# Performance work log

Hardware: AMD Instinct MI355X
Metric: run time of the kernel (lower is better)

Reference implementation:

```python
import jax, jax.numpy as jnp
import numpy as np

R_CUT = 2.5
N_BASIS = 8
BOX_SIZE = 10.0


def radial_encode(r, n, r_cut):
    """Gaussian radial basis on squared distance r: (...,) -> (..., n).
    Centers spread over [0, r_cut], width r_cut/n. (Helper source not given;
    this is the standard RBF encode used in such MD graph nets.)"""
    mu = jnp.linspace(0.0, r_cut, n, dtype=r.dtype)        # (n,)
    sigma = r_cut / n
    d = r[..., None] - mu                                   # (..., n)
    return jnp.exp(-0.5 * (d / sigma) ** 2)


def setup_inputs() -> dict:
    key = jax.random.key(0)
    k1, k2 = jax.random.split(key)
    batch, nodes, deg = 8, 20000, 32
    pos = jax.random.uniform(k1, (batch, nodes, 3), dtype=jnp.float32) * BOX_SIZE
    box = jnp.full((3,), BOX_SIZE, dtype=jnp.float32)
    nbr_idx = jax.random.randint(k2, (nodes, deg), 0, nodes, dtype=jnp.int64)
    return {"pos": pos, "box": box, "nbr_idx": nbr_idx}


def reference(pos, box, nbr_idx):
    # pos: (B, N, 3); box: (3,); nbr_idx: (N, deg)
    ang_box = box / (2.0 * jnp.pi)                          # (3,)
    # edges_read: gather neighbor positions -> (B, N, deg, 3)
    nbr_pos = pos[:, nbr_idx]                               # (B, N, deg, 3)
    edges = nbr_pos - pos[:, :, None]                       # relative displacement
    # periodic-box sin wrap
    edges = ang_box * jnp.sin(edges / ang_box)
    r = jnp.sum(edges ** 2, axis=-1)                        # (B, N, deg) squared dist
    x = radial_encode(r, N_BASIS, R_CUT)                    # (B, N, deg, 8)
    xv = x[..., None] * edges[..., None, :]                 # (B, N, deg, 8, 3) outer product
    # edges_reduce: sum over neighbor axis
    y = jnp.sum(x, axis=2)                                  # (B, N, 8)
    yv = jnp.sum(xv, axis=2)                                # (B, N, 8, 3)
    return (y, yv)
```

## Files before the change

### kernel.cpp

```cpp
#include <hip/hip_runtime.h>

static constexpr int BATCH = 8;
static constexpr int NODES = 20000;
static constexpr int DEG   = 32;
static constexpr int NB    = 8;

#if defined(__has_builtin) && __has_builtin(__builtin_amdgcn_exp2f)
#define EXP2F(x) __builtin_amdgcn_exp2f(x)
#else
#define EXP2F(x) exp2f(x)
#endif

static constexpr float C1 = -7.3865986f;
static constexpr float C2 = 5.2761417f;

__global__ __launch_bounds__(256)
void transpose_pos_kernel(const float* __restrict__ pos, float4* __restrict__ pos_t) {
    const int t = blockIdx.x * blockDim.x + threadIdx.x;
    if (t >= BATCH * NODES) return;
    const int b = t / NODES;
    const int i = t - b * NODES;
    pos_t[(size_t)i * BATCH + b] =
        make_float4(pos[3 * t + 0], pos[3 * t + 1], pos[3 * t + 2], 0.0f);
}

__global__ __launch_bounds__(256)
void graph_embed_kernel(const float4* __restrict__ pos_t,
                        const float* __restrict__ box,
                        const int*   __restrict__ nbr,
                        float* __restrict__ out)
{
    const int t = blockIdx.x * blockDim.x + threadIdx.x;
    if (t >= BATCH * NODES) return;
    const int i = t >> 3;
    const int b = t & 7;

    const float inv2pi = 0.15915494309189535f;
    const float ab0 = box[0] * inv2pi;
    const float ab1 = box[1] * inv2pi;
    const float ab2 = box[2] * inv2pi;
    const float ia0 = 1.0f / ab0;
    const float ia1 = 1.0f / ab1;
    const float ia2 = 1.0f / ab2;

    float h[NB - 1];
#pragma unroll
    for (int k = 0; k < NB - 1; ++k)
        h[k] = __expf(-0.6530612245f * (float)(2 * k + 1));

    const float4 p = pos_t[(size_t)i * BATCH + b];

    float y0[NB], v0[NB], v1[NB], v2[NB];
#pragma unroll
    for (int k = 0; k < NB; ++k) { y0[k] = 0.f; v0[k] = 0.f; v1[k] = 0.f; v2[k] = 0.f; }

    const int4* __restrict__ row = (const int4*)(nbr + (size_t)i * DEG);

    int4 idx = row[0];
    float4 q0 = pos_t[(size_t)idx.x * BATCH + b];
    float4 q1 = pos_t[(size_t)idx.y * BATCH + b];
    float4 q2 = pos_t[(size_t)idx.z * BATCH + b];
    float4 q3 = pos_t[(size_t)idx.w * BATCH + b];

#pragma unroll
    for (int grp = 0; grp < DEG / 4; ++grp) {
        float4 n0, n1, n2, n3;
        if (grp + 1 < DEG / 4) {
            const int4 nidx = row[grp + 1];
            n0 = pos_t[(size_t)nidx.x * BATCH + b];
            n1 = pos_t[(size_t)nidx.y * BATCH + b];
            n2 = pos_t[(size_t)nidx.z * BATCH + b];
            n3 = pos_t[(size_t)nidx.w * BATCH + b];
        }
        const float4 qs[4] = { q0, q1, q2, q3 };
#pragma unroll
        for (int jj = 0; jj < 4; ++jj) {
            const float4 q = qs[jj];
            const float e0 = ab0 * __sinf((q.x - p.x) * ia0);
            const float e1 = ab1 * __sinf((q.y - p.y) * ia1);
            const float e2 = ab2 * __sinf((q.z - p.z) * ia2);
            const float r  = fmaf(e0, e0, fmaf(e1, e1, e2 * e2));

            const float g = EXP2F(r * C2);
            float x = EXP2F(r * r * C1);
#pragma unroll
            for (int k = 0; k < NB; ++k) {
                y0[k] += x;
                v0[k] = fmaf(x, e0, v0[k]);
                v1[k] = fmaf(x, e1, v1[k]);
                v2[k] = fmaf(x, e2, v2[k]);
                if (k < NB - 1) x = x * g * h[k];
            }
        }
        q0 = n0; q1 = n1; q2 = n2; q3 = n3;
    }

    const size_t ot = (size_t)b * NODES + i;
    float* __restrict__ yptr = out + ot * NB;
    *(float4*)(yptr + 0) = make_float4(y0[0], y0[1], y0[2], y0[3]);
    *(float4*)(yptr + 4) = make_float4(y0[4], y0[5], y0[6], y0[7]);

    float* __restrict__ vptr = out + (size_t)BATCH * NODES * NB + ot * (NB * 3);
    *(float4*)(vptr +  0) = make_float4(v0[0], v1[0], v2[0], v0[1]);
    *(float4*)(vptr +  4) = make_float4(v1[1], v2[1], v0[2], v1[2]);
    *(float4*)(vptr +  8) = make_float4(v2[2], v0[3], v1[3], v2[3]);
    *(float4*)(vptr + 12) = make_float4(v0[4], v1[4], v2[4], v0[5]);
    *(float4*)(vptr + 16) = make_float4(v1[5], v2[5], v0[6], v1[6]);
    *(float4*)(vptr + 20) = make_float4(v2[6], v0[7], v1[7], v2[7]);
}

__global__ __launch_bounds__(256)
void graph_embed_fallback_kernel(const float* __restrict__ pos,
                                 const float* __restrict__ box,
                                 const int*   __restrict__ nbr,
                                 float* __restrict__ out)
{
    const int t = blockIdx.x * blockDim.x + threadIdx.x;
    if (t >= BATCH * NODES) return;
    const int b = t / NODES;
    const int i = t - b * NODES;

    const float inv2pi = 0.15915494309189535f;
    const float ab0 = box[0] * inv2pi, ab1 = box[1] * inv2pi, ab2 = box[2] * inv2pi;
    const float ia0 = 1.0f / ab0, ia1 = 1.0f / ab1, ia2 = 1.0f / ab2;

    float h[NB - 1];
#pragma unroll
    for (int k = 0; k < NB - 1; ++k)
        h[k] = __expf(-0.6530612245f * (float)(2 * k + 1));

    const float* __restrict__ pb = pos + (size_t)b * NODES * 3;
    const float p0 = pb[3 * i + 0], p1 = pb[3 * i + 1], p2 = pb[3 * i + 2];

    float y0[NB], v0[NB], v1[NB], v2[NB];
#pragma unroll
    for (int k = 0; k < NB; ++k) { y0[k] = 0.f; v0[k] = 0.f; v1[k] = 0.f; v2[k] = 0.f; }

    const int* __restrict__ row = nbr + (size_t)i * DEG;
#pragma unroll 4
    for (int j = 0; j < DEG; ++j) {
        const int idx = row[j];
        const float* __restrict__ q = pb + (size_t)idx * 3;
        const float e0 = ab0 * __sinf((q[0] - p0) * ia0);
        const float e1 = ab1 * __sinf((q[1] - p1) * ia1);
        const float e2 = ab2 * __sinf((q[2] - p2) * ia2);
        const float r  = fmaf(e0, e0, fmaf(e1, e1, e2 * e2));
        const float g = EXP2F(r * C2);
        float x = EXP2F(r * r * C1);
#pragma unroll
        for (int k = 0; k < NB; ++k) {
            y0[k] += x;
            v0[k] = fmaf(x, e0, v0[k]);
            v1[k] = fmaf(x, e1, v1[k]);
            v2[k] = fmaf(x, e2, v2[k]);
            if (k < NB - 1) x = x * g * h[k];
        }
    }

    float* __restrict__ yptr = out + (size_t)t * NB;
    *(float4*)(yptr + 0) = make_float4(y0[0], y0[1], y0[2], y0[3]);
    *(float4*)(yptr + 4) = make_float4(y0[4], y0[5], y0[6], y0[7]);
    float* __restrict__ vptr = out + (size_t)BATCH * NODES * NB + (size_t)t * (NB * 3);
    *(float4*)(vptr +  0) = make_float4(v0[0], v1[0], v2[0], v0[1]);
    *(float4*)(vptr +  4) = make_float4(v1[1], v2[1], v0[2], v1[2]);
    *(float4*)(vptr +  8) = make_float4(v2[2], v0[3], v1[3], v2[3]);
    *(float4*)(vptr + 12) = make_float4(v0[4], v1[4], v2[4], v0[5]);
    *(float4*)(vptr + 16) = make_float4(v1[5], v2[5], v0[6], v1[6]);
    *(float4*)(vptr + 20) = make_float4(v2[6], v0[7], v1[7], v2[7]);
}

extern "C" void kernel_launch(void* const* d_in, const int* in_sizes, int n_in,
                              void* d_out, int out_size, void* d_ws, size_t ws_size,
                              hipStream_t stream) {
    const float* pos = (const float*)d_in[0];
    const float* box = (const float*)d_in[1];
    const int*   nbr = (const int*)d_in[2];
    float* out = (float*)d_out;

    const int total = BATCH * NODES;
    const int block = 256;
    const int grid  = (total + block - 1) / block;

    const size_t packed_bytes = (size_t)total * sizeof(float4);
    if (ws_size >= packed_bytes) {
        float4* pos_t = (float4*)d_ws;
        transpose_pos_kernel<<<grid, block, 0, stream>>>(pos, pos_t);
        graph_embed_kernel<<<grid, block, 0, stream>>>(pos_t, box, nbr, out);
    } else {
        graph_embed_fallback_kernel<<<grid, block, 0, stream>>>(pos, box, nbr, out);
    }
}
```

Before: 87.96 us.

## Split neighbor loop across two lanes and stage outputs through LDS for coalesced stores

Each (node, batch) pair is now handled by two threads, each covering half of the 32 neighbors, with a cross-lane shuffle reduction; this doubles the thread count to raise parallelism and latency hiding for the gathers. Results are staged in shared memory per block of 16 nodes and written out as contiguous float4 rows, replacing scattered per-thread strided stores to the batch-major output. A launch_bounds occupancy hint is added. The cost is extra shuffles, LDS traffic and a block barrier, plus per-thread setup that is now done twice as often.

```diff
diff --git a/kernel.cpp b/kernel.cpp
--- a/kernel.cpp
+++ b/kernel.cpp
@@ -24,16 +24,22 @@
         make_float4(pos[3 * t + 0], pos[3 * t + 1], pos[3 * t + 2], 0.0f);
 }
 
-__global__ __launch_bounds__(256)
+__global__ __launch_bounds__(256, 4)
 void graph_embed_kernel(const float4* __restrict__ pos_t,
                         const float* __restrict__ box,
                         const int*   __restrict__ nbr,
                         float* __restrict__ out)
 {
-    const int t = blockIdx.x * blockDim.x + threadIdx.x;
-    if (t >= BATCH * NODES) return;
-    const int i = t >> 3;
-    const int b = t & 7;
+    __shared__ float y_lds[8 * 132];
+    __shared__ float yv_lds[8 * 388];
+
+    const int tid = threadIdx.x;
+    const int t   = blockIdx.x * 256 + tid;
+    const int b   = t & 7;
+    const int jh  = (t >> 3) & 1;
+    const int i   = t >> 4;
+    const int i_sub  = tid >> 4;
+    const int i_base = blockIdx.x * 16;
 
     const float inv2pi = 0.15915494309189535f;
     const float ab0 = box[0] * inv2pi;
@@ -54,23 +60,24 @@
 #pragma unroll
     for (int k = 0; k < NB; ++k) { y0[k] = 0.f; v0[k] = 0.f; v1[k] = 0.f; v2[k] = 0.f; }
 
-    const int4* __restrict__ row = (const int4*)(nbr + (size_t)i * DEG);
-
-    int4 idx = row[0];
-    float4 q0 = pos_t[(size_t)idx.x * BATCH + b];
-    float4 q1 = pos_t[(size_t)idx.y * BATCH + b];
-    float4 q2 = pos_t[(size_t)idx.z * BATCH + b];
-    float4 q3 = pos_t[(size_t)idx.w * BATCH + b];
-
-#pragma unroll
-    for (int grp = 0; grp < DEG / 4; ++grp) {
+    const int4* __restrict__ row4 = (const int4*)(nbr + (size_t)i * DEG) + jh * 4;
+    const int4 rr0 = row4[0], rr1 = row4[1], rr2 = row4[2], rr3 = row4[3];
+    const int4 rr[4] = { rr0, rr1, rr2, rr3 };
+
+    float4 q0 = pos_t[(size_t)rr[0].x * BATCH + b];
+    float4 q1 = pos_t[(size_t)rr[0].y * BATCH + b];
+    float4 q2 = pos_t[(size_t)rr[0].z * BATCH + b];
+    float4 q3 = pos_t[(size_t)rr[0].w * BATCH + b];
+
+#pragma unroll
+    for (int g = 0; g < 4; ++g) {
         float4 n0, n1, n2, n3;
-        if (grp + 1 < DEG / 4) {
-            const int4 nidx = row[grp + 1];
-            n0 = pos_t[(size_t)nidx.x * BATCH + b];
-            n1 = pos_t[(size_t)nidx.y * BATCH + b];
-            n2 = pos_t[(size_t)nidx.z * BATCH + b];
-            n3 = pos_t[(size_t)nidx.w * BATCH + b];
+        if (g + 1 < 4) {
+            const int4 nx = rr[g + 1];
+            n0 = pos_t[(size_t)nx.x * BATCH + b];
+            n1 = pos_t[(size_t)nx.y * BATCH + b];
+            n2 = pos_t[(size_t)nx.z * BATCH + b];
+            n3 = pos_t[(size_t)nx.w * BATCH + b];
         }
         const float4 qs[4] = { q0, q1, q2, q3 };
 #pragma unroll
@@ -81,7 +88,7 @@
             const float e2 = ab2 * __sinf((q.z - p.z) * ia2);
             const float r  = fmaf(e0, e0, fmaf(e1, e1, e2 * e2));
 
-            const float g = EXP2F(r * C2);
+            const float g2 = EXP2F(r * C2);
             float x = EXP2F(r * r * C1);
 #pragma unroll
             for (int k = 0; k < NB; ++k) {
@@ -89,24 +96,48 @@
                 v0[k] = fmaf(x, e0, v0[k]);
                 v1[k] = fmaf(x, e1, v1[k]);
                 v2[k] = fmaf(x, e2, v2[k]);
-                if (k < NB - 1) x = x * g * h[k];
+                if (k < NB - 1) x = x * g2 * h[k];
             }
         }
         q0 = n0; q1 = n1; q2 = n2; q3 = n3;
     }
 
-    const size_t ot = (size_t)b * NODES + i;
-    float* __restrict__ yptr = out + ot * NB;
-    *(float4*)(yptr + 0) = make_float4(y0[0], y0[1], y0[2], y0[3]);
-    *(float4*)(yptr + 4) = make_float4(y0[4], y0[5], y0[6], y0[7]);
-
-    float* __restrict__ vptr = out + (size_t)BATCH * NODES * NB + ot * (NB * 3);
-    *(float4*)(vptr +  0) = make_float4(v0[0], v1[0], v2[0], v0[1]);
-    *(float4*)(vptr +  4) = make_float4(v1[1], v2[1], v0[2], v1[2]);
-    *(float4*)(vptr +  8) = make_float4(v2[2], v0[3], v1[3], v2[3]);
-    *(float4*)(vptr + 12) = make_float4(v0[4], v1[4], v2[4], v0[5]);
-    *(float4*)(vptr + 16) = make_float4(v1[5], v2[5], v0[6], v1[6]);
-    *(float4*)(vptr + 20) = make_float4(v2[6], v0[7], v1[7], v2[7]);
+#pragma unroll
+    for (int k = 0; k < NB; ++k) {
+        y0[k] += __shfl_xor(y0[k], 8);
+        v0[k] += __shfl_xor(v0[k], 8);
+        v1[k] += __shfl_xor(v1[k], 8);
+        v2[k] += __shfl_xor(v2[k], 8);
+    }
+
+    if ((tid & 8) == 0) {
+        float* yl = y_lds + b * 132 + i_sub * 8;
+        float* vl = yv_lds + b * 388 + i_sub * 24;
+#pragma unroll
+        for (int k = 0; k < NB; ++k) {
+            yl[k] = y0[k];
+            vl[k * 3 + 0] = v0[k];
+            vl[k * 3 + 1] = v1[k];
+            vl[k * 3 + 2] = v2[k];
+        }
+    }
+    __syncthreads();
+
+    {
+        const int bb  = tid >> 5;
+        const int off = tid & 31;
+        *(float4*)(out + (size_t)(bb * NODES + i_base) * NB + off * 4) =
+            *(const float4*)(y_lds + bb * 132 + off * 4);
+    }
+    float* __restrict__ outv = out + (size_t)BATCH * NODES * NB;
+#pragma unroll
+    for (int s = 0; s < 3; ++s) {
+        const int idx = tid + s * 256;
+        const int bb  = idx / 96;
+        const int rem = idx - bb * 96;
+        *(float4*)(outv + (size_t)(bb * NODES + i_base) * (NB * 3) + rem * 4) =
+            *(const float4*)(yv_lds + bb * 388 + rem * 4);
+    }
 }
 
 __global__ __launch_bounds__(256)
@@ -178,15 +209,14 @@
     float* out = (float*)d_out;
 
     const int total = BATCH * NODES;
-    const int block = 256;
-    const int grid  = (total + block - 1) / block;
-
     const size_t packed_bytes = (size_t)total * sizeof(float4);
     if (ws_size >= packed_bytes) {
         float4* pos_t = (float4*)d_ws;
-        transpose_pos_kernel<<<grid, block, 0, stream>>>(pos, pos_t);
-        graph_embed_kernel<<<grid, block, 0, stream>>>(pos_t, box, nbr, out);
+        const int block = 256;
+        transpose_pos_kernel<<<(total + block - 1) / block, block, 0, stream>>>(pos, pos_t);
+        graph_embed_kernel<<<(total * 2) / block, block, 0, stream>>>(pos_t, box, nbr, out);
     } else {
-        graph_embed_fallback_kernel<<<grid, block, 0, stream>>>(pos, box, nbr, out);
-    }
-}
+        const int block = 256;
+        graph_embed_fallback_kernel<<<(total + block - 1) / block, block, 0, stream>>>(pos, box, nbr, out);
+    }
+}
```

Result: faster. 83.94 us (-4.6%).
